# Optimization experiments

Measured on AMD Instinct MI355X. Metric: run time of the kernel, lower is better.

The kernel has to match this reference:

```python
import jax, jax.numpy as jnp
import numpy as np

N_KNOTS = 10
NC = 32
BATCH = 32
EPS = 1e-5

def _spline_matrix(n):
    step = 1.0 / (n - 1.0)
    mat = 4 * np.eye(n - 2)
    np.fill_diagonal(mat[1:, :-1], 1)
    np.fill_diagonal(mat[:-1, 1:], 1)
    A = 6 * np.linalg.inv(mat) / step ** 2
    z = np.zeros(n - 2)
    A = np.vstack([z, A, z])            # [n, n-2]
    B = np.zeros((n - 2, n))
    np.fill_diagonal(B, 1)
    np.fill_diagonal(B[:, 1:], -2)
    np.fill_diagonal(B[:, 2:], 1)
    return np.dot(A, B).astype(np.float32)  # [n, n]

def setup_inputs() -> dict:
    key = jax.random.key(0)
    ks = jax.random.split(key, 8)
    n, nc = N_KNOTS, NC
    inp = {}
    inp['batch'] = jax.random.uniform(ks[0], (BATCH, 3, 256, 256), dtype=jnp.float32)
    chans = [3, nc, 2 * nc, 4 * nc, 8 * nc, 16 * nc]
    for i in range(5):
        ci, co = chans[i], chans[i + 1]
        inp['c%d_w' % (i + 1)] = jax.random.normal(jax.random.fold_in(ks[1], i), (co, ci, 3, 3), dtype=jnp.float32) * 0.1
        inp['c%d_b' % (i + 1)] = jnp.zeros((co,), jnp.float32)
        inp['bn%d_g' % (i + 1)] = jnp.ones((co,), jnp.float32)
        inp['bn%d_b' % (i + 1)] = jnp.zeros((co,), jnp.float32)
    inp['l1_w'] = jax.random.normal(ks[2], (100 * n, 16 * nc * 7 * 7), dtype=jnp.float32) * 0.02
    inp['l1_b'] = jnp.zeros((100 * n,), jnp.float32)
    inp['l2_w'] = jax.random.normal(ks[3], (3 * n, 100 * n), dtype=jnp.float32) * 0.02
    inp['l2_b'] = jnp.zeros((3 * n,), jnp.float32)
    inp['matrix'] = jnp.asarray(_spline_matrix(n))
    return inp

def _conv_bn(x, w, b, g, be):
    # conv (stride 2, VALID) -> relu -> batchnorm (training-mode batch stats)
    y = jax.lax.conv_general_dilated(x, w, (2, 2), 'VALID', dimension_numbers=('NCHW', 'OIHW', 'NCHW'))
    y = jax.nn.relu(y + b[None, :, None, None])
    m = jnp.mean(y, axis=(0, 2, 3))
    v = jnp.var(y, axis=(0, 2, 3))
    inv = jax.lax.rsqrt(v + EPS)
    return g[None, :, None, None] * (y - m[None, :, None, None]) * inv[None, :, None, None] + be[None, :, None, None]

def _forward(batch, c1_w, c1_b, bn1_g, bn1_b, c2_w, c2_b, bn2_g, bn2_b,
             c3_w, c3_b, bn3_g, bn3_b, c4_w, c4_b, bn4_g, bn4_b,
             c5_w, c5_b, bn5_g, bn5_b, l1_w, l1_b, l2_w, l2_b, matrix):
    n = matrix.shape[0]
    h = 1.0 / (n - 1.0)  # knot spacing (self.step)
    B, _, H, W = batch.shape

    x = _conv_bn(batch, c1_w, c1_b, bn1_g, bn1_b)
    x = _conv_bn(x, c2_w, c2_b, bn2_g, bn2_b)
    x = _conv_bn(x, c3_w, c3_b, bn3_g, bn3_b)
    x = _conv_bn(x, c4_w, c4_b, bn4_g, bn4_b)
    x = _conv_bn(x, c5_w, c5_b, bn5_g, bn5_b)
    x = x.reshape(B, -1)
    x = jax.nn.relu(x @ l1_w.T + l1_b)
    x = x @ l2_w.T + l2_b
    ys = x.reshape(B, 3, n) / 100.0

    identity = jnp.arange(n, dtype=batch.dtype) / (n - 1)
    ys_aug = ys + identity                                    # [B,3,n]
    # second-derivative values M at knots (natural cubic spline solve as dense matmul)
    M = jnp.einsum('ij,bcj->bci', matrix, ys_aug)             # [B,3,n]
    a = (M[..., 1:] - M[..., :-1]) / (6 * h)                  # [B,3,n-1]
    b_ = M[..., :-1] / 2
    c_ = (ys_aug[..., 1:] - ys_aug[..., :-1]) / h - (M[..., 1:] + 2 * M[..., :-1]) * (h / 6)
    d_ = ys_aug[..., :-1]

    def eval_spline(xv):  # xv: [B,3,K] -> [B,3,K]; gather segment coeffs instead of one-hot matmul
        xi = jnp.clip(jnp.floor(xv / h), 0, n - 2).astype(jnp.int32)
        xf = xv - xi.astype(xv.dtype) * h
        ag = jnp.take_along_axis(a, xi, axis=-1)
        bg = jnp.take_along_axis(b_, xi, axis=-1)
        cg = jnp.take_along_axis(c_, xi, axis=-1)
        dg = jnp.take_along_axis(d_, xi, axis=-1)
        return ((ag * xf + bg) * xf + cg) * xf + dg

    out = eval_spline(batch.reshape(B, 3, H * W)).reshape(B, 3, H, W)
    vals = jnp.arange(255, dtype=batch.dtype) / 255.0          # arange(0,1,1/255)
    splines = eval_spline(jnp.broadcast_to(vals, (B, 3, 255)))
    return out, splines

def reference(batch, c1_w, c1_b, bn1_g, bn1_b, c2_w, c2_b, bn2_g, bn2_b,
              c3_w, c3_b, bn3_g, bn3_b, c4_w, c4_b, bn4_g, bn4_b,
              c5_w, c5_b, bn5_g, bn5_b, l1_w, l1_b, l2_w, l2_b, matrix):
    return _forward(batch, c1_w, c1_b, bn1_g, bn1_b, c2_w, c2_b, bn2_g, bn2_b,
                    c3_w, c3_b, bn3_g, bn3_b, c4_w, c4_b, bn4_g, bn4_b,
                    c5_w, c5_b, bn5_g, bn5_b, l1_w, l1_b, l2_w, l2_b, matrix)
```

## Files before the change

### kernel.cpp

```cpp
#include <hip/hip_runtime.h>
#include <hip/hip_bf16.h>

#define BEPS 1e-5f
#define FC1_KS 98
#define FC1_KC 256
#define C1NB 2017
#define STS 512

typedef __attribute__((ext_vector_type(8))) short short8v;
typedef __attribute__((ext_vector_type(4))) float f32x4;
typedef unsigned short ushort_t;

__device__ __forceinline__ float bf2f(ushort_t u) {
    unsigned int x = ((unsigned int)u) << 16;
    return __builtin_bit_cast(float, x);
}
__device__ __forceinline__ ushort_t f2bf(float v) {
    __hip_bfloat16 h = __float2bfloat16(v);
    return *(ushort_t*)&h;
}

__global__ __launch_bounds__(256) void conv1_direct(
    const float* __restrict__ in, const float* __restrict__ w,
    const float* __restrict__ bias, ushort_t* __restrict__ out) {
    __shared__ float ws[864];
    __shared__ float bs[32];
    const int tid = threadIdx.x;
    for (int i = tid; i < 864; i += 256) ws[i] = w[i];
    if (tid < 32) bs[tid] = bias[tid];
    __syncthreads();

    const int TOT = 32 * 16129;
    int p = blockIdx.x * 256 + tid;
    if (p >= TOT) return;
    int b = p / 16129, pp = p - b * 16129;
    int i = pp / 127, j = pp - i * 127;
    const float* ib = in + ((long long)b * 3) * 65536 + (2 * i) * 256 + 2 * j;
    float patch[27];
#pragma unroll
    for (int ci = 0; ci < 3; ++ci)
#pragma unroll
        for (int di = 0; di < 3; ++di) {
            const float* rp = ib + ci * 65536 + di * 256;
            float2 v01 = *(const float2*)rp;
            patch[ci * 9 + di * 3 + 0] = v01.x;
            patch[ci * 9 + di * 3 + 1] = v01.y;
            patch[ci * 9 + di * 3 + 2] = rp[2];
        }

    ushort_t res[32];
#pragma unroll
    for (int co = 0; co < 32; co += 4) {
        float a0 = bs[co], a1 = bs[co + 1], a2 = bs[co + 2], a3 = bs[co + 3];
#pragma unroll
        for (int t = 0; t < 27; ++t) {
            float pv = patch[t];
            a0 = fmaf(pv, ws[(co + 0) * 27 + t], a0);
            a1 = fmaf(pv, ws[(co + 1) * 27 + t], a1);
            a2 = fmaf(pv, ws[(co + 2) * 27 + t], a2);
            a3 = fmaf(pv, ws[(co + 3) * 27 + t], a3);
        }
        res[co + 0] = f2bf(fmaxf(a0, 0.f));
        res[co + 1] = f2bf(fmaxf(a1, 0.f));
        res[co + 2] = f2bf(fmaxf(a2, 0.f));
        res[co + 3] = f2bf(fmaxf(a3, 0.f));
    }
    ushort_t* ob = out + (long long)p * 32;
#pragma unroll
    for (int v = 0; v < 4; ++v)
        *(short8v*)&ob[v * 8] = *(const short8v*)&res[v * 8];
}

__global__ __launch_bounds__(256) void conv_mfma(
    const ushort_t* __restrict__ in, const ushort_t* __restrict__ wf,
    const float* __restrict__ effb, ushort_t* __restrict__ out,
    float* __restrict__ pacc, float* __restrict__ spart,
    int B, int Ci, int lgCi, int Hi, int Wi, int Co, int Ho, int Wo,
    int K, int Kp, int kcount, int Spart) {
    const int HoWo = Ho * Wo;
    const int N = B * HoWo;
    __shared__ __align__(16) ushort_t As[64 * 64];
    __shared__ __align__(16) ushort_t Bs[128 * 64];
    const int tid = threadIdx.x;
    const int m0 = blockIdx.y * 64;
    const int n0 = blockIdx.x * 128;
    const int kbeg = blockIdx.z * kcount;

    const int rowA = tid >> 2;
    const int kqA = (tid & 3) * 16;
    const ushort_t* wrowA = wf + (long long)(m0 + rowA) * Kp + kbeg + kqA;
    const int swA = (rowA & 7) << 3;
    const int rowB = tid >> 1;
    const int kqB = (tid & 1) * 32;
    const int n = n0 + rowB;
    const int nn = (n < N) ? n : (N - 1);
    const int pb = nn / HoWo, pp = nn - pb * HoWo;
    const int pi = pp / Wo, pj = pp - pi * Wo;
    const long long base0 = ((long long)pb * Hi + 2 * pi) * Wi + 2 * pj;
    const int swB = (rowB & 7) << 3;

    const int w = tid >> 6;
    const int lane = tid & 63;
    const int wco = (w >> 1) * 32, wpx = (w & 1) * 64;
    const int lm = lane & 15, lk = lane >> 4;

    short8v rA0, rA1, rB[4];
    rA0 = *(const short8v*)(wrowA);
    rA1 = *(const short8v*)(wrowA + 8);
#pragma unroll
    for (int ch = 0; ch < 2; ++ch) {
        int c16 = kqB + ch * 16;
        int kg = kbeg + c16;
        int tap = kg >> lgCi;
        tap = tap > 8 ? 8 : tap;
        int ci0 = kg & (Ci - 1);
        int dy = tap / 3, dx = tap - dy * 3;
        const ushort_t* src = in + (base0 + dy * Wi + dx) * Ci + ci0;
        rB[ch * 2] = *(const short8v*)src;
        rB[ch * 2 + 1] = *(const short8v*)(src + 8);
    }

    f32x4 acc[2][4] = {};
    for (int k0 = 0; k0 < kcount; k0 += 64) {
        *(short8v*)&As[rowA * 64 + ((kqA + 0) ^ swA)] = rA0;
        *(short8v*)&As[rowA * 64 + ((kqA + 8) ^ swA)] = rA1;
#pragma unroll
        for (int ch = 0; ch < 2; ++ch) {
            int c16 = kqB + ch * 16;
            *(short8v*)&Bs[rowB * 64 + ((c16 + 0) ^ swB)] = rB[ch * 2];
            *(short8v*)&Bs[rowB * 64 + ((c16 + 8) ^ swB)] = rB[ch * 2 + 1];
        }
        __syncthreads();
        int k1 = k0 + 64;
        if (k1 < kcount) {
            rA0 = *(const short8v*)(wrowA + k1);
            rA1 = *(const short8v*)(wrowA + k1 + 8);
#pragma unroll
            for (int ch = 0; ch < 2; ++ch) {
                int c16 = kqB + ch * 16;
                int kg = kbeg + k1 + c16;
                int tap = kg >> lgCi;
                tap = tap > 8 ? 8 : tap;
                int ci0 = kg & (Ci - 1);
                int dy = tap / 3, dx = tap - dy * 3;
                const ushort_t* src = in + (base0 + dy * Wi + dx) * Ci + ci0;
                rB[ch * 2] = *(const short8v*)src;
                rB[ch * 2 + 1] = *(const short8v*)(src + 8);
            }
        }
#pragma unroll
        for (int kk = 0; kk < 2; ++kk) {
            const int kb = kk * 32 + lk * 8;
            const int ra0 = wco + lm, ra1 = wco + 16 + lm;
            short8v a0 = *(const short8v*)&As[ra0 * 64 + (kb ^ ((ra0 & 7) << 3))];
            short8v a1 = *(const short8v*)&As[ra1 * 64 + (kb ^ ((ra1 & 7) << 3))];
            const int rb0 = wpx + lm, rb1 = wpx + 16 + lm;
            const int rb2 = wpx + 32 + lm, rb3 = wpx + 48 + lm;
            short8v b0 = *(const short8v*)&Bs[rb0 * 64 + (kb ^ ((rb0 & 7) << 3))];
            short8v b1 = *(const short8v*)&Bs[rb1 * 64 + (kb ^ ((rb1 & 7) << 3))];
            short8v b2 = *(const short8v*)&Bs[rb2 * 64 + (kb ^ ((rb2 & 7) << 3))];
            short8v b3 = *(const short8v*)&Bs[rb3 * 64 + (kb ^ ((rb3 & 7) << 3))];
            acc[0][0] = __builtin_amdgcn_mfma_f32_16x16x32_bf16(a0, b0, acc[0][0], 0, 0, 0);
            acc[0][1] = __builtin_amdgcn_mfma_f32_16x16x32_bf16(a0, b1, acc[0][1], 0, 0, 0);
            acc[0][2] = __builtin_amdgcn_mfma_f32_16x16x32_bf16(a0, b2, acc[0][2], 0, 0, 0);
            acc[0][3] = __builtin_amdgcn_mfma_f32_16x16x32_bf16(a0, b3, acc[0][3], 0, 0, 0);
            acc[1][0] = __builtin_amdgcn_mfma_f32_16x16x32_bf16(a1, b0, acc[1][0], 0, 0, 0);
            acc[1][1] = __builtin_amdgcn_mfma_f32_16x16x32_bf16(a1, b1, acc[1][1], 0, 0, 0);
            acc[1][2] = __builtin_amdgcn_mfma_f32_16x16x32_bf16(a1, b2, acc[1][2], 0, 0, 0);
            acc[1][3] = __builtin_amdgcn_mfma_f32_16x16x32_bf16(a1, b3, acc[1][3], 0, 0, 0);
        }
        __syncthreads();
    }
    if (pacc) {
        float* pbuf = pacc + ((long long)blockIdx.z * N) * Co;
#pragma unroll
        for (int nb = 0; nb < 4; ++nb) {
            int np = n0 + wpx + nb * 16 + lm;
            if (np >= N) continue;
#pragma unroll
            for (int amr = 0; amr < 2; ++amr) {
                int cobase = m0 + wco + amr * 16 + lk * 4;
                float4 vv = make_float4(acc[amr][nb][0], acc[amr][nb][1],
                                        acc[amr][nb][2], acc[amr][nb][3]);
                *(float4*)&pbuf[(long long)np * Co + cobase] = vv;
            }
        }
    } else {
        float ssum[2][4] = {}, ssq[2][4] = {};
#pragma unroll
        for (int nb = 0; nb < 4; ++nb) {
            int np = n0 + wpx + nb * 16 + lm;
            bool val = (np < N);
#pragma unroll
            for (int amr = 0; amr < 2; ++amr) {
                int cobase = m0 + wco + amr * 16 + lk * 4;
                float4 eb = *(const float4*)&effb[cobase];
                float v0 = fmaxf(acc[amr][nb][0] + eb.x, 0.f);
                float v1 = fmaxf(acc[amr][nb][1] + eb.y, 0.f);
                float v2 = fmaxf(acc[amr][nb][2] + eb.z, 0.f);
                float v3 = fmaxf(acc[amr][nb][3] + eb.w, 0.f);
                if (val) {
                    ushort4 u;
                    u.x = f2bf(v0); u.y = f2bf(v1); u.z = f2bf(v2); u.w = f2bf(v3);
                    *(ushort4*)&out[(long long)np * Co + cobase] = u;
                    ssum[amr][0] += v0; ssq[amr][0] = fmaf(v0, v0, ssq[amr][0]);
                    ssum[amr][1] += v1; ssq[amr][1] = fmaf(v1, v1, ssq[amr][1]);
                    ssum[amr][2] += v2; ssq[amr][2] = fmaf(v2, v2, ssq[amr][2]);
                    ssum[amr][3] += v3; ssq[amr][3] = fmaf(v3, v3, ssq[amr][3]);
                }
            }
        }
#pragma unroll
        for (int mm = 1; mm < 16; mm <<= 1) {
#pragma unroll
            for (int amr = 0; amr < 2; ++amr)
#pragma unroll
                for (int r = 0; r < 4; ++r) {
                    ssum[amr][r] += __shfl_xor(ssum[amr][r], mm, 64);
                    ssq[amr][r] += __shfl_xor(ssq[amr][r], mm, 64);
                }
        }
        __shared__ float lss[4][32], lsq[4][32];
        if (lm == 0) {
#pragma unroll
            for (int amr = 0; amr < 2; ++amr)
#pragma unroll
                for (int r = 0; r < 4; ++r) {
                    lss[w][amr * 16 + lk * 4 + r] = ssum[amr][r];
                    lsq[w][amr * 16 + lk * 4 + r] = ssq[amr][r];
                }
        }
        __syncthreads();
        if (tid < 64) {
            int half = tid >> 5, c32 = tid & 31;
            float s = lss[half * 2][c32] + lss[half * 2 + 1][c32];
            float q = lsq[half * 2][c32] + lsq[half * 2 + 1][c32];
            int c = m0 + half * 32 + c32;
            spart[((long long)c * Spart + blockIdx.x) * 2 + 0] = s;
            spart[((long long)c * Spart + blockIdx.x) * 2 + 1] = q;
        }
    }
}

__global__ __launch_bounds__(256) void convz_stats(
    const float* __restrict__ pacc, const float* __restrict__ effb,
    ushort_t* __restrict__ out, float* __restrict__ part,
    long long total, int Co, int Z) {
    const int tid = threadIdx.x;
    const int c0 = (tid * 8) & (Co - 1);
    float eb[8];
    {
        float4 e0 = *(const float4*)&effb[c0];
        float4 e1 = *(const float4*)&effb[c0 + 4];
        eb[0] = e0.x; eb[1] = e0.y; eb[2] = e0.z; eb[3] = e0.w;
        eb[4] = e1.x; eb[5] = e1.y; eb[6] = e1.z; eb[7] = e1.w;
    }
    float sum[8] = {}, sq[8] = {};
    const long long nchunk = total >> 11;
    for (long long g = blockIdx.x; g < nchunk; g += 512) {
        long long off = (g << 11) + tid * 8;
        float v[8];
#pragma unroll
        for (int j = 0; j < 8; ++j) v[j] = eb[j];
        for (int z = 0; z < Z; ++z) {
            const float* pz = pacc + (long long)z * total + off;
            float4 a = *(const float4*)pz;
            float4 b2 = *(const float4*)(pz + 4);
            v[0] += a.x; v[1] += a.y; v[2] += a.z; v[3] += a.w;
            v[4] += b2.x; v[5] += b2.y; v[6] += b2.z; v[7] += b2.w;
        }
        short8v o;
#pragma unroll
        for (int j = 0; j < 8; ++j) {
            float r = fmaxf(v[j], 0.f);
            o[j] = (short)f2bf(r);
            sum[j] += r;
            sq[j] = fmaf(r, r, sq[j]);
        }
        *(short8v*)&out[off] = o;
    }
    __shared__ float rs[256][8], rq[256][8];
#pragma unroll
    for (int j = 0; j < 8; ++j) { rs[tid][j] = sum[j]; rq[tid][j] = sq[j]; }
    __syncthreads();
    const int G = Co >> 3;
    const int TPG = 256 / G;
    for (int c = tid; c < Co; c += 256) {
        int grp = c >> 3, j = c & 7;
        float s = 0.f, q = 0.f;
        for (int i = 0; i < TPG; ++i) {
            s += rs[grp + i * G][j];
            q += rq[grp + i * G][j];
        }
        part[(c * 512 + blockIdx.x) * 2 + 0] = s;
        part[(c * 512 + blockIdx.x) * 2 + 1] = q;
    }
}

__global__ __launch_bounds__(256) void stats_flat(
    const ushort_t* __restrict__ y, float* __restrict__ part,
    long long total, int C, int S) {
    const int tid = threadIdx.x;
    float sum[8] = {}, sq[8] = {};
    const long long nchunk = (total + 2047) >> 11;
    for (long long g = blockIdx.x; g < nchunk; g += S) {
        long long off = (g << 11) + tid * 8;
        if (off + 8 <= total) {
            short8v v8 = *(const short8v*)(y + off);
#pragma unroll
            for (int j = 0; j < 8; ++j) {
                float v = bf2f((ushort_t)v8[j]);
                sum[j] += v;
                sq[j] = fmaf(v, v, sq[j]);
            }
        }
    }
    __shared__ float rs[256][8], rq[256][8];
#pragma unroll
    for (int j = 0; j < 8; ++j) { rs[tid][j] = sum[j]; rq[tid][j] = sq[j]; }
    __syncthreads();
    const int G = C >> 3;
    const int TPG = 256 / G;
    for (int c = tid; c < C; c += 256) {
        int grp = c >> 3, j = c & 7;
        float s = 0.f, q = 0.f;
        for (int i = 0; i < TPG; ++i) {
            s += rs[grp + i * G][j];
            q += rq[grp + i * G][j];
        }
        part[(c * S + blockIdx.x) * 2 + 0] = s;
        part[(c * S + blockIdx.x) * 2 + 1] = q;
    }
}

__global__ __launch_bounds__(256) void stats_final_w(
    const float* __restrict__ part, const float* __restrict__ g,
    const float* __restrict__ be, float* __restrict__ scale,
    float* __restrict__ shift, int C, int S, float invN) {
    int c = blockIdx.x * 4 + (threadIdx.x >> 6);
    int lane = threadIdx.x & 63;
    if (c >= C) return;
    float s = 0.f, q = 0.f;
    for (int i = lane; i < S; i += 64) {
        s += part[((long long)c * S + i) * 2 + 0];
        q += part[((long long)c * S + i) * 2 + 1];
    }
#pragma unroll
    for (int off = 32; off > 0; off >>= 1) {
        s += __shfl_down(s, off, 64);
        q += __shfl_down(q, off, 64);
    }
    if (lane == 0) {
        float m = s * invN;
        float v = q * invN - m * m;
        float inv = rsqrtf(v + BEPS);
        float sc = g[c] * inv;
        scale[c] = sc;
        shift[c] = be[c] - m * sc;
    }
}

__global__ __launch_bounds__(256) void fold_fused(
    const float* __restrict__ w, const float* __restrict__ scale,
    const float* __restrict__ shift, const float* __restrict__ bias,
    ushort_t* __restrict__ wout, float* __restrict__ effb,
    int Ci, int lgCi, int K, int Kp, int Co, int WB) {
    if ((int)blockIdx.x < WB) {
        int idx = blockIdx.x * 256 + threadIdx.x;
        if (idx >= Co * Kp) return;
        int co = idx / Kp, k = idx - co * Kp;
        ushort_t o = 0;
        if (k < K) {
            int tap = k >> lgCi;
            int ci = k & (Ci - 1);
            o = f2bf(w[((long long)co * Ci + ci) * 9 + tap] * scale[ci]);
        }
        wout[idx] = o;
    } else {
        int co = ((int)blockIdx.x - WB) * 4 + (threadIdx.x >> 6);
        int lane = threadIdx.x & 63;
        if (co >= Co) return;
        const int CK = Ci * 9;
        const float* wr = w + (long long)co * CK;
        float acc = 0.f;
        for (int k = lane; k < CK; k += 64) acc = fmaf(wr[k], shift[k / 9], acc);
#pragma unroll
        for (int off = 32; off > 0; off >>= 1) acc += __shfl_down(acc, off, 64);
        if (lane == 0) effb[co] = acc + bias[co];
    }
}

__global__ void bn_apply_x(const ushort_t* __restrict__ y, const float* __restrict__ scale,
                           const float* __restrict__ shift, ushort_t* __restrict__ xB) {
    int idx = blockIdx.x * blockDim.x + threadIdx.x;
    if (idx >= 802816) return;
    int b = idx / 25088, k = idx - b * 25088;
    int c = k / 49, p = k - c * 49;
    float v = bf2f(y[((long long)b * 49 + p) * 512 + c]);
    xB[idx] = f2bf(fmaf(v, scale[c], shift[c]));
}

__global__ __launch_bounds__(256) void fc1_mfma(
    const float* __restrict__ w, const ushort_t* __restrict__ xB,
    float* __restrict__ part) {
    const int K = 25088;
    __shared__ __align__(16) ushort_t As[64 * 256];
    __shared__ __align__(16) ushort_t Bs[32 * 256];
    const int tid = threadIdx.x;
    const int m0 = blockIdx.y * 64;
    const int kbeg = blockIdx.x * FC1_KC;

    {
        const int r = tid >> 2;
        const int kq = (tid & 3) * 64;
        const int m = m0 + r;
        const bool mv = (m < 1000);
        const float* wr = w + (long long)m * K + kbeg + kq;
        const int sw = (r & 7) << 3;
#pragma unroll
        for (int g = 0; g < 8; ++g) {
            short8v o = {0, 0, 0, 0, 0, 0, 0, 0};
            if (mv) {
                float4 f0 = *(const float4*)(wr + g * 8);
                float4 f1 = *(const float4*)(wr + g * 8 + 4);
                o[0] = (short)f2bf(f0.x); o[1] = (short)f2bf(f0.y);
                o[2] = (short)f2bf(f0.z); o[3] = (short)f2bf(f0.w);
                o[4] = (short)f2bf(f1.x); o[5] = (short)f2bf(f1.y);
                o[6] = (short)f2bf(f1.z); o[7] = (short)f2bf(f1.w);
            }
            *(short8v*)&As[r * 256 + ((kq + g * 8) ^ sw)] = o;
        }
    }
    {
        const int b = tid >> 3;
        const int kq = (tid & 7) * 32;
        const ushort_t* xr = xB + (long long)b * K + kbeg + kq;
        const int sw = (b & 7) << 3;
#pragma unroll
        for (int g = 0; g < 4; ++g) {
            short8v v = *(const short8v*)(xr + g * 8);
            *(short8v*)&Bs[b * 256 + ((kq + g * 8) ^ sw)] = v;
        }
    }
    __syncthreads();
    const int wv = tid >> 6, lane = tid & 63;
    const int lm = lane & 15, lk = lane >> 4;
    const int wm = wv * 16;
    f32x4 acc0 = {}, acc1 = {};
    const int ra = wm + lm;
    const int swa = (ra & 7) << 3;
    const int swb = (lm & 7) << 3;
#pragma unroll
    for (int s = 0; s < 8; ++s) {
        int kb = s * 32 + lk * 8;
        short8v av = *(const short8v*)&As[ra * 256 + (kb ^ swa)];
        short8v b0 = *(const short8v*)&Bs[lm * 256 + (kb ^ swb)];
        short8v b1 = *(const short8v*)&Bs[(16 + lm) * 256 + (kb ^ swb)];
        acc0 = __builtin_amdgcn_mfma_f32_16x16x32_bf16(av, b0, acc0, 0, 0, 0);
        acc1 = __builtin_amdgcn_mfma_f32_16x16x32_bf16(av, b1, acc1, 0, 0, 0);
    }
    float* pb = part + ((long long)blockIdx.y * FC1_KS + blockIdx.x) * 2048;
#pragma unroll
    for (int r = 0; r < 4; ++r) {
        pb[(wm + lk * 4 + r) * 32 + lm] = acc0[r];
        pb[(wm + lk * 4 + r) * 32 + 16 + lm] = acc1[r];
    }
}

__global__ void fc1_reduce(const float* __restrict__ part, const float* __restrict__ bias,
                           float* __restrict__ z) {
    int idx = blockIdx.x * blockDim.x + threadIdx.x;
    if (idx >= 32000) return;
    int o = idx >> 5, b = idx & 31;
    int mt = o >> 6, mr = o & 63;
    const float* p = part + ((long long)mt * FC1_KS) * 2048 + mr * 32 + b;
    float s0 = 0.f, s1 = 0.f;
    int ks = 0;
    for (; ks + 1 < FC1_KS; ks += 2) {
        s0 += p[(long long)ks * 2048];
        s1 += p[(long long)(ks + 1) * 2048];
    }
    for (; ks < FC1_KS; ++ks) s0 += p[(long long)ks * 2048];
    z[b * 1000 + o] = fmaxf(s0 + s1 + bias[o], 0.f);
}

__global__ __launch_bounds__(256) void fc2_v2(const float* __restrict__ z,
                                              const float* __restrict__ w,
                                              const float* __restrict__ bias,
                                              float* __restrict__ ys) {
    int gid = blockIdx.x * 4 + (threadIdx.x >> 6);
    int lane = threadIdx.x & 63;
    if (gid >= 960) return;
    int b = gid / 30, o = gid - b * 30;
    const float* zr = z + (long long)b * 1000;
    const float* wr = w + (long long)o * 1000;
    float acc = 0.f;
    for (int k = lane; k < 1000; k += 64) acc = fmaf(zr[k], wr[k], acc);
    for (int off = 32; off > 0; off >>= 1) acc += __shfl_down(acc, off, 64);
    if (lane == 0) ys[gid] = acc + bias[o];
}

__global__ void spline_coeff(const float* __restrict__ ysraw, const float* __restrict__ matrix,
                             float4* __restrict__ coef) {
    int r = threadIdx.x;
    if (r >= 96) return;
    const float h = 1.0f / 9.0f;
    float ya[10];
    int b = r / 3, ch = r % 3;
#pragma unroll
    for (int j = 0; j < 10; ++j)
        ya[j] = ysraw[b * 30 + ch * 10 + j] / 100.0f + (float)j / 9.0f;
    float M[10];
#pragma unroll
    for (int i = 0; i < 10; ++i) {
        float acc = 0.f;
#pragma unroll
        for (int j = 0; j < 10; ++j) acc = fmaf(matrix[i * 10 + j], ya[j], acc);
        M[i] = acc;
    }
#pragma unroll
    for (int k = 0; k < 9; ++k) {
        float a = (M[k + 1] - M[k]) / (6.0f * h);
        float bb = M[k] * 0.5f;
        float cc = (ya[k + 1] - ya[k]) / h - (M[k + 1] + 2.0f * M[k]) * (h / 6.0f);
        float dd = ya[k];
        coef[r * 9 + k] = make_float4(a, bb, cc, dd);
    }
}

__global__ void eval_all(const float4* __restrict__ batch4, const float4* __restrict__ coef,
                         float4* __restrict__ out4, float* __restrict__ outt) {
    int idx = blockIdx.x * blockDim.x + threadIdx.x;
    const float h = 1.0f / 9.0f;
    if (idx < 1572864) {
        int plane = idx >> 14;
        float4 xv4 = batch4[idx];
        float xin[4] = {xv4.x, xv4.y, xv4.z, xv4.w};
        float xout[4];
#pragma unroll
        for (int e = 0; e < 4; ++e) {
            float xv = xin[e];
            int xi = (int)floorf(xv / h);
            xi = min(max(xi, 0), 8);
            float xf = xv - (float)xi * h;
            float4 cf = coef[plane * 9 + xi];
            xout[e] = fmaf(fmaf(fmaf(cf.x, xf, cf.y), xf, cf.z), xf, cf.w);
        }
        out4[idx] = make_float4(xout[0], xout[1], xout[2], xout[3]);
    } else {
        int t = idx - 1572864;
        if (t >= 96 * 255) return;
        int plane = t / 255;
        int j = t - plane * 255;
        float xv = (float)j / 255.0f;
        int xi = (int)floorf(xv / h);
        xi = min(max(xi, 0), 8);
        float xf = xv - (float)xi * h;
        float4 cf = coef[plane * 9 + xi];
        outt[t] = fmaf(fmaf(fmaf(cf.x, xf, cf.y), xf, cf.z), xf, cf.w);
    }
}

extern "C" void kernel_launch(void* const* d_in, const int* in_sizes, int n_in,
                              void* d_out, int out_size, void* d_ws, size_t ws_size,
                              hipStream_t stream) {
    const int B = 32;
    const float* batch = (const float*)d_in[0];
    const float* cw[5] = {(const float*)d_in[1], (const float*)d_in[5], (const float*)d_in[9],
                          (const float*)d_in[13], (const float*)d_in[17]};
    const float* cb[5] = {(const float*)d_in[2], (const float*)d_in[6], (const float*)d_in[10],
                          (const float*)d_in[14], (const float*)d_in[18]};
    const float* bg[5] = {(const float*)d_in[3], (const float*)d_in[7], (const float*)d_in[11],
                          (const float*)d_in[15], (const float*)d_in[19]};
    const float* bb[5] = {(const float*)d_in[4], (const float*)d_in[8], (const float*)d_in[12],
                          (const float*)d_in[16], (const float*)d_in[20]};
    const float* l1w = (const float*)d_in[21];
    const float* l1b = (const float*)d_in[22];
    const float* l2w = (const float*)d_in[23];
    const float* l2b = (const float*)d_in[24];
    const float* matrix = (const float*)d_in[25];

    float* f = (float*)d_ws;
    const size_t A_F = 8258048;
    const size_t Bq_F = 4064256;
    const size_t W_F = 589824;
    ushort_t* bufA = (ushort_t*)f;
    ushort_t* bufB = (ushort_t*)(f + A_F);
    ushort_t* Wf_bf = (ushort_t*)(f + A_F + Bq_F);
    float* effb  = f + A_F + Bq_F + W_F;
    float* scale = effb + 512;
    float* shift = scale + 512;
    float* part  = shift + 512;
    float* x5    = part + 524288;
    float* pacc  = x5 + 802816;
    float* z1    = pacc + 3686400;
    float* ysb   = z1 + 32000;
    float4* coef = (float4*)(ysb + 960);

    const int Ci[5]   = {3, 32, 64, 128, 256};
    const int lgCi[5] = {0, 5, 6, 7, 8};
    const int Co[5]   = {32, 64, 128, 256, 512};
    const int Hi[5]   = {256, 127, 63, 31, 15};
    const int Ho[5]   = {127, 63, 31, 15, 7};
    const int Zl[5]   = {1, 1, 1, 1, 3};

    ushort_t* bufs[2] = {bufA, bufB};

    conv1_direct<<<C1NB, 256, 0, stream>>>(batch, cw[0], cb[0], bufA);
    {
        long long total = (long long)B * 16129 * 32;
        stats_flat<<<STS, 256, 0, stream>>>(bufA, part, total, 32, STS);
        stats_final_w<<<8, 256, 0, stream>>>(part, bg[0], bb[0], scale, shift, 32, STS,
                                             1.0f / (float)(B * 16129));
    }

    const ushort_t* cur = bufA;
    for (int l = 1; l < 5; ++l) {
        ushort_t* outb = bufs[l % 2];
        int K = Ci[l] * 9;
        int Kp = (K + 63) & ~63;
        int WB = (Co[l] * Kp + 255) / 256;
        int BBk = (Co[l] + 3) / 4;
        fold_fused<<<WB + BBk, 256, 0, stream>>>(cw[l], scale, shift, cb[l], Wf_bf, effb,
                                                 Ci[l], lgCi[l], K, Kp, Co[l], WB);
        int N = B * Ho[l] * Ho[l];
        int Z = Zl[l];
        int kcount = Kp / Z;
        dim3 grid((N + 127) / 128, Co[l] / 64, Z);
        if (Z == 1) {
            conv_mfma<<<grid, 256, 0, stream>>>(cur, Wf_bf, effb, outb, nullptr, part,
                                                B, Ci[l], lgCi[l], Hi[l], Hi[l], Co[l],
                                                Ho[l], Ho[l], K, Kp, kcount, grid.x);
            stats_final_w<<<(Co[l] + 3) / 4, 256, 0, stream>>>(
                part, bg[l], bb[l], scale, shift, Co[l], grid.x, 1.0f / (float)N);
        } else {
            conv_mfma<<<grid, 256, 0, stream>>>(cur, Wf_bf, effb, nullptr, pacc, nullptr,
                                                B, Ci[l], lgCi[l], Hi[l], Hi[l], Co[l],
                                                Ho[l], Ho[l], K, Kp, kcount, 0);
            long long total = (long long)N * Co[l];
            convz_stats<<<512, 256, 0, stream>>>(pacc, effb, outb, part, total, Co[l], Z);
            stats_final_w<<<(Co[l] + 3) / 4, 256, 0, stream>>>(
                part, bg[l], bb[l], scale, shift, Co[l], 512, 1.0f / (float)N);
        }
        cur = outb;
    }

    ushort_t* xB = (ushort_t*)x5;
    bn_apply_x<<<(802816 + 255) / 256, 256, 0, stream>>>(cur, scale, shift, xB);
    {
        dim3 grid(FC1_KS, 16);
        fc1_mfma<<<grid, 256, 0, stream>>>(l1w, xB, pacc);
    }
    fc1_reduce<<<(32000 + 255) / 256, 256, 0, stream>>>(pacc, l1b, z1);
    fc2_v2<<<240, 256, 0, stream>>>(z1, l2w, l2b, ysb);
    spline_coeff<<<1, 96, 0, stream>>>(ysb, matrix, coef);

    float* out = (float*)d_out;
    int evtot = 1572864 + 96 * 255;
    eval_all<<<(evtot + 255) / 256, 256, 0, stream>>>((const float4*)batch, coef,
                                                      (float4*)out, out + 6291456);
}
```

Baseline: 238.3 us.

## Fuse conv1 BN statistics into conv1 and spline coefficients into eval kernel

Conv1 now reduces per-channel sum and sum-of-squares for each block in shared memory and writes per-block partials directly. This removes the separate stats_flat pass that re-read the whole conv1 bf16 output. The spline coefficient computation is folded into eval_all, so every block rebuilds the 96x9 coefficient table in LDS instead of running a single-block kernel first. This drops launches and a large memory pass, but it raises conv1's LDS use, which may lower occupancy, and adds redundant per-block setup work before the memory-bound evaluation.

Result: no change. 237.3 us (-0.4%).

```diff
diff --git a/kernel.cpp b/kernel.cpp
--- a/kernel.cpp
+++ b/kernel.cpp
@@ -22,9 +22,12 @@
 
 __global__ __launch_bounds__(256) void conv1_direct(
     const float* __restrict__ in, const float* __restrict__ w,
-    const float* __restrict__ bias, ushort_t* __restrict__ out) {
+    const float* __restrict__ bias, ushort_t* __restrict__ out,
+    float* __restrict__ part) {
     __shared__ float ws[864];
     __shared__ float bs[32];
+    __shared__ float tp[256 * 36];
+    __shared__ float ps[8][32], pq[8][32];
     const int tid = threadIdx.x;
     for (int i = tid; i < 864; i += 256) ws[i] = w[i];
     if (tid < 32) bs[tid] = bias[tid];
@@ -32,8 +35,9 @@
 
     const int TOT = 32 * 16129;
     int p = blockIdx.x * 256 + tid;
-    if (p >= TOT) return;
-    int b = p / 16129, pp = p - b * 16129;
+    const bool valid = (p < TOT);
+    int pc = valid ? p : (TOT - 1);
+    int b = pc / 16129, pp = pc - b * 16129;
     int i = pp / 127, j = pp - i * 127;
     const float* ib = in + ((long long)b * 3) * 65536 + (2 * i) * 256 + 2 * j;
     float patch[27];
@@ -48,7 +52,7 @@
             patch[ci * 9 + di * 3 + 2] = rp[2];
         }
 
-    ushort_t res[32];
+    float vals[32];
 #pragma unroll
     for (int co = 0; co < 32; co += 4) {
         float a0 = bs[co], a1 = bs[co + 1], a2 = bs[co + 2], a3 = bs[co + 3];
@@ -60,15 +64,48 @@
             a2 = fmaf(pv, ws[(co + 2) * 27 + t], a2);
             a3 = fmaf(pv, ws[(co + 3) * 27 + t], a3);
         }
-        res[co + 0] = f2bf(fmaxf(a0, 0.f));
-        res[co + 1] = f2bf(fmaxf(a1, 0.f));
-        res[co + 2] = f2bf(fmaxf(a2, 0.f));
-        res[co + 3] = f2bf(fmaxf(a3, 0.f));
-    }
-    ushort_t* ob = out + (long long)p * 32;
-#pragma unroll
-    for (int v = 0; v < 4; ++v)
-        *(short8v*)&ob[v * 8] = *(const short8v*)&res[v * 8];
+        vals[co + 0] = fmaxf(a0, 0.f);
+        vals[co + 1] = fmaxf(a1, 0.f);
+        vals[co + 2] = fmaxf(a2, 0.f);
+        vals[co + 3] = fmaxf(a3, 0.f);
+    }
+    if (valid) {
+        ushort_t res[32];
+#pragma unroll
+        for (int c = 0; c < 32; ++c) res[c] = f2bf(vals[c]);
+        ushort_t* ob = out + (long long)p * 32;
+#pragma unroll
+        for (int v = 0; v < 4; ++v)
+            *(short8v*)&ob[v * 8] = *(const short8v*)&res[v * 8];
+    } else {
+#pragma unroll
+        for (int c = 0; c < 32; ++c) vals[c] = 0.f;
+    }
+#pragma unroll
+    for (int v = 0; v < 8; ++v)
+        *(float4*)&tp[tid * 36 + v * 4] = make_float4(vals[v * 4], vals[v * 4 + 1],
+                                                      vals[v * 4 + 2], vals[v * 4 + 3]);
+    __syncthreads();
+    {
+        const int c = tid & 31, s = tid >> 5;
+        float sm = 0.f, sq = 0.f;
+#pragma unroll 8
+        for (int q = 0; q < 32; ++q) {
+            float v = tp[(s * 32 + q) * 36 + c];
+            sm += v;
+            sq = fmaf(v, v, sq);
+        }
+        ps[s][c] = sm;
+        pq[s][c] = sq;
+    }
+    __syncthreads();
+    if (tid < 32) {
+        float sm = 0.f, sq = 0.f;
+#pragma unroll
+        for (int s = 0; s < 8; ++s) { sm += ps[s][tid]; sq += pq[s][tid]; }
+        part[((long long)tid * C1NB + blockIdx.x) * 2 + 0] = sm;
+        part[((long long)tid * C1NB + blockIdx.x) * 2 + 1] = sq;
+    }
 }
 
 __global__ __launch_bounds__(256) void conv_mfma(
@@ -297,42 +334,6 @@
     }
 }
 
-__global__ __launch_bounds__(256) void stats_flat(
-    const ushort_t* __restrict__ y, float* __restrict__ part,
-    long long total, int C, int S) {
-    const int tid = threadIdx.x;
-    float sum[8] = {}, sq[8] = {};
-    const long long nchunk = (total + 2047) >> 11;
-    for (long long g = blockIdx.x; g < nchunk; g += S) {
-        long long off = (g << 11) + tid * 8;
-        if (off + 8 <= total) {
-            short8v v8 = *(const short8v*)(y + off);
-#pragma unroll
-            for (int j = 0; j < 8; ++j) {
-                float v = bf2f((ushort_t)v8[j]);
-                sum[j] += v;
-                sq[j] = fmaf(v, v, sq[j]);
-            }
-        }
-    }
-    __shared__ float rs[256][8], rq[256][8];
-#pragma unroll
-    for (int j = 0; j < 8; ++j) { rs[tid][j] = sum[j]; rq[tid][j] = sq[j]; }
-    __syncthreads();
-    const int G = C >> 3;
-    const int TPG = 256 / G;
-    for (int c = tid; c < C; c += 256) {
-        int grp = c >> 3, j = c & 7;
-        float s = 0.f, q = 0.f;
-        for (int i = 0; i < TPG; ++i) {
-            s += rs[grp + i * G][j];
-            q += rq[grp + i * G][j];
-        }
-        part[(c * S + blockIdx.x) * 2 + 0] = s;
-        part[(c * S + blockIdx.x) * 2 + 1] = q;
-    }
-}
-
 __global__ __launch_bounds__(256) void stats_final_w(
     const float* __restrict__ part, const float* __restrict__ g,
     const float* __restrict__ be, float* __restrict__ scale,
@@ -500,38 +501,41 @@
     if (lane == 0) ys[gid] = acc + bias[o];
 }
 
-__global__ void spline_coeff(const float* __restrict__ ysraw, const float* __restrict__ matrix,
-                             float4* __restrict__ coef) {
-    int r = threadIdx.x;
-    if (r >= 96) return;
+__global__ __launch_bounds__(256) void eval_all(
+    const float4* __restrict__ batch4, const float* __restrict__ ysraw,
+    const float* __restrict__ matrix, float4* __restrict__ out4,
+    float* __restrict__ outt) {
+    __shared__ float mat[100];
+    __shared__ float4 coefs[864];
+    const int tid = threadIdx.x;
     const float h = 1.0f / 9.0f;
-    float ya[10];
-    int b = r / 3, ch = r % 3;
-#pragma unroll
-    for (int j = 0; j < 10; ++j)
-        ya[j] = ysraw[b * 30 + ch * 10 + j] / 100.0f + (float)j / 9.0f;
-    float M[10];
-#pragma unroll
-    for (int i = 0; i < 10; ++i) {
-        float acc = 0.f;
-#pragma unroll
-        for (int j = 0; j < 10; ++j) acc = fmaf(matrix[i * 10 + j], ya[j], acc);
-        M[i] = acc;
-    }
-#pragma unroll
-    for (int k = 0; k < 9; ++k) {
-        float a = (M[k + 1] - M[k]) / (6.0f * h);
-        float bb = M[k] * 0.5f;
-        float cc = (ya[k + 1] - ya[k]) / h - (M[k + 1] + 2.0f * M[k]) * (h / 6.0f);
-        float dd = ya[k];
-        coef[r * 9 + k] = make_float4(a, bb, cc, dd);
-    }
-}
-
-__global__ void eval_all(const float4* __restrict__ batch4, const float4* __restrict__ coef,
-                         float4* __restrict__ out4, float* __restrict__ outt) {
-    int idx = blockIdx.x * blockDim.x + threadIdx.x;
-    const float h = 1.0f / 9.0f;
+    if (tid < 100) mat[tid] = matrix[tid];
+    __syncthreads();
+    if (tid < 96) {
+        int b = tid / 3, ch = tid - b * 3;
+        float ya[10];
+#pragma unroll
+        for (int j = 0; j < 10; ++j)
+            ya[j] = ysraw[b * 30 + ch * 10 + j] / 100.0f + (float)j / 9.0f;
+        float M[10];
+#pragma unroll
+        for (int i = 0; i < 10; ++i) {
+            float acc = 0.f;
+#pragma unroll
+            for (int j = 0; j < 10; ++j) acc = fmaf(mat[i * 10 + j], ya[j], acc);
+            M[i] = acc;
+        }
+#pragma unroll
+        for (int k = 0; k < 9; ++k) {
+            float a = (M[k + 1] - M[k]) / (6.0f * h);
+            float bb = M[k] * 0.5f;
+            float cc = (ya[k + 1] - ya[k]) / h - (M[k + 1] + 2.0f * M[k]) * (h / 6.0f);
+            float dd = ya[k];
+            coefs[tid * 9 + k] = make_float4(a, bb, cc, dd);
+        }
+    }
+    __syncthreads();
+    int idx = blockIdx.x * 256 + tid;
     if (idx < 1572864) {
         int plane = idx >> 14;
         float4 xv4 = batch4[idx];
@@ -543,21 +547,22 @@
             int xi = (int)floorf(xv / h);
             xi = min(max(xi, 0), 8);
             float xf = xv - (float)xi * h;
-            float4 cf = coef[plane * 9 + xi];
+            float4 cf = coefs[plane * 9 + xi];
             xout[e] = fmaf(fmaf(fmaf(cf.x, xf, cf.y), xf, cf.z), xf, cf.w);
         }
         out4[idx] = make_float4(xout[0], xout[1], xout[2], xout[3]);
     } else {
         int t = idx - 1572864;
-        if (t >= 96 * 255) return;
-        int plane = t / 255;
-        int j = t - plane * 255;
-        float xv = (float)j / 255.0f;
-        int xi = (int)floorf(xv / h);
-        xi = min(max(xi, 0), 8);
-        float xf = xv - (float)xi * h;
-        float4 cf = coef[plane * 9 + xi];
-        outt[t] = fmaf(fmaf(fmaf(cf.x, xf, cf.y), xf, cf.z), xf, cf.w);
+        if (t < 96 * 255) {
+            int plane = t / 255;
+            int j = t - plane * 255;
+            float xv = (float)j / 255.0f;
+            int xi = (int)floorf(xv / h);
+            xi = min(max(xi, 0), 8);
+            float xf = xv - (float)xi * h;
+            float4 cf = coefs[plane * 9 + xi];
+            outt[t] = fmaf(fmaf(fmaf(cf.x, xf, cf.y), xf, cf.z), xf, cf.w);
+        }
     }
 }
 
@@ -595,7 +600,6 @@
     float* pacc  = x5 + 802816;
     float* z1    = pacc + 3686400;
     float* ysb   = z1 + 32000;
-    float4* coef = (float4*)(ysb + 960);
 
     const int Ci[5]   = {3, 32, 64, 128, 256};
     const int lgCi[5] = {0, 5, 6, 7, 8};
@@ -606,13 +610,9 @@
 
     ushort_t* bufs[2] = {bufA, bufB};
 
-    conv1_direct<<<C1NB, 256, 0, stream>>>(batch, cw[0], cb[0], bufA);
-    {
-        long long total = (long long)B * 16129 * 32;
-        stats_flat<<<STS, 256, 0, stream>>>(bufA, part, total, 32, STS);
-        stats_final_w<<<8, 256, 0, stream>>>(part, bg[0], bb[0], scale, shift, 32, STS,
-                                             1.0f / (float)(B * 16129));
-    }
+    conv1_direct<<<C1NB, 256, 0, stream>>>(batch, cw[0], cb[0], bufA, part);
+    stats_final_w<<<8, 256, 0, stream>>>(part, bg[0], bb[0], scale, shift, 32, C1NB,
+                                         1.0f / (float)(B * 16129));
 
     const ushort_t* cur = bufA;
     for (int l = 1; l < 5; ++l) {
@@ -653,10 +653,9 @@
     }
     fc1_reduce<<<(32000 + 255) / 256, 256, 0, stream>>>(pacc, l1b, z1);
     fc2_v2<<<240, 256, 0, stream>>>(z1, l2w, l2b, ysb);
-    spline_coeff<<<1, 96, 0, stream>>>(ysb, matrix, coef);
 
     float* out = (float*)d_out;
     int evtot = 1572864 + 96 * 255;
-    eval_all<<<(evtot + 255) / 256, 256, 0, stream>>>((const float4*)batch, coef,
+    eval_all<<<(evtot + 255) / 256, 256, 0, stream>>>((const float4*)batch, ysb, matrix,
                                                       (float4*)out, out + 6291456);
 }
```
